# Optimization experiments

Hardware: AMD Instinct MI355X
Metric: run time of the kernel (lower is better)

The kernel has to match this reference:

```python
import math
import jax, jax.numpy as jnp
import numpy as np

H_HEADS = 8
SR = 2


def _layernorm(x, w, b, eps=1e-5):
    mu = jnp.mean(x, axis=-1, keepdims=True)
    var = jnp.mean((x - mu) ** 2, axis=-1, keepdims=True)
    return (x - mu) / jnp.sqrt(var + eps) * w + b


def _dwconv(x, w, b, pad, stride=1):
    # x: (B,C,H,W), w: (C,1,kh,kw) depthwise
    y = jax.lax.conv_general_dilated(
        x, w, (stride, stride), padding=pad,
        dimension_numbers=('NCHW', 'OIHW', 'NCHW'),
        feature_group_count=x.shape[1])
    return y + b[None, :, None, None]


def _lpu(x, w3, b3, w51, b51, w15, b15):
    # LocalPerceptionUint (act=False): x + dw3x3(x) + dw1x5(dw5x1(x))
    out = _dwconv(x, w3, b3, [(1, 1), (1, 1)])
    out2 = _dwconv(_dwconv(x, w51, b51, [(2, 2), (0, 0)]), w15, b15, [(0, 0), (2, 2)])
    return x + out + out2


def _split_halves(x, B, C, N, h, w):
    # faithful to torch: permute(0,2,1).reshape(B,C,N//2,2) then per-slice permute+reshape
    x_ = x.transpose(0, 2, 1).reshape(B, C, N // 2, 2)
    x1 = x_[..., 0].transpose(0, 2, 1).reshape(B, C, h, w)
    x2 = x_[..., 1].transpose(0, 2, 1).reshape(B, C, h, w)
    return x1, x2


def reference(x, ln_in_w, ln_in_b, ln_out_w, ln_out_b,
              lpu1_w3, lpu1_b3, lpu1_w51, lpu1_b51, lpu1_w15, lpu1_b15,
              lpu2_w3, lpu2_b3, lpu2_w51, lpu2_b51, lpu2_w15, lpu2_b15,
              q_w, q_b, kv_w, kv_b, proj_w, proj_b,
              sr1_w, sr1_b, sr2_w, sr2_b, sa_norm_w, sa_norm_b,
              mlp_w1, mlp_b1, mlp_w2, mlp_b2):
    B, N, C = x.shape
    h = int(math.isqrt(N // 2)); w = h
    dh = C // H_HEADS

    # ---- LPU on two interleaved halves ----
    x1, x2 = _split_halves(x, B, C, N, h, w)
    x1 = x1 + _lpu(x1, lpu1_w3, lpu1_b3, lpu1_w51, lpu1_b51, lpu1_w15, lpu1_b15)
    x2 = x2 + _lpu(x2, lpu2_w3, lpu2_b3, lpu2_w51, lpu2_b51, lpu2_w15, lpu2_b15)
    x = jnp.concatenate([x1, x2], axis=2).reshape(B, C, -1).transpose(0, 2, 1)  # (B,N,C)

    # ---- SelfAttention on LayerNorm(x) ----
    xa = _layernorm(x, ln_in_w, ln_in_b)
    q = (xa @ q_w.T + q_b).reshape(B, N, H_HEADS, dh).transpose(0, 2, 1, 3)  # (B,H,N,dh)

    xs1, xs2 = _split_halves(xa, B, C, N, h, w)
    xcat = jnp.concatenate([xs1, xs2], axis=2)  # (B,C,2h,w)
    pad = SR // 2
    xshift = jnp.pad(xcat, ((0, 0), (0, 0), (pad, 0), (pad, 0)))  # top/left pad
    y1 = _dwconv(xcat, sr1_w, sr1_b, [(0, 0), (0, 0)], stride=SR)
    y2 = _dwconv(xshift, sr2_w, sr2_b, [(0, 0), (0, 0)], stride=SR)
    Hs, Ws = y1.shape[2], y1.shape[3]
    y2 = y2[:, :, :Hs, :Ws]
    xk = jnp.stack([y1.reshape(B, C, -1), y2.reshape(B, C, -1)], axis=3)
    xk = xk.reshape(B, C, -1).transpose(0, 2, 1)  # (B, Nk, C), interleaved
    xk = _layernorm(xk, sa_norm_w, sa_norm_b)
    kv = (xk @ kv_w.T + kv_b).reshape(B, -1, 2, H_HEADS, dh).transpose(2, 0, 3, 1, 4)
    k, v = kv[0], kv[1]  # (B,H,Nk,dh)

    attn = jnp.einsum('bhnd,bhmd->bhnm', q, k) * (dh ** -0.5)
    M = attn.shape[-1]
    if 101 < M < 10000:  # static shape -> Python branch, matches torch gate
        topk = int(M * 0.8)
        idx = jax.lax.top_k(attn, topk)[1]  # (B,H,N,topk)
        bi = jnp.arange(B)[:, None, None, None]
        hi = jnp.arange(H_HEADS)[None, :, None, None]
        ni = jnp.arange(N)[None, None, :, None]
        mask = jnp.zeros(attn.shape, dtype=bool).at[bi, hi, ni, idx].set(True)
        attn = jnp.where(mask, attn, -jnp.inf)
    attn = jax.nn.softmax(attn, axis=-1)
    sa = jnp.einsum('bhnm,bhmd->bhnd', attn, v).transpose(0, 2, 1, 3).reshape(B, N, C)
    sa = sa @ proj_w.T + proj_b

    x = x + sa
    xm = _layernorm(x, ln_out_w, ln_out_b)
    hid = jax.nn.gelu(xm @ mlp_w1.T + mlp_b1, approximate=False)
    x = x + (hid @ mlp_w2.T + mlp_b2)
    return x


def setup_inputs():
    C = 512
    E = 4
    ks = iter(jax.random.split(jax.random.key(0), 24))

    def w(shape, std=0.02):
        return jax.random.normal(next(ks), shape, jnp.float32) * std

    inp = {"x": jax.random.normal(next(ks), (4, 2048, C), jnp.float32)}
    for nm in ("ln_in", "ln_out", "sa_norm"):
        inp[nm + "_w"] = jnp.ones((C,), jnp.float32)
        inp[nm + "_b"] = jnp.zeros((C,), jnp.float32)
    for p in ("lpu1", "lpu2"):
        inp[p + "_w3"] = w((C, 1, 3, 3))
        inp[p + "_b3"] = jnp.zeros((C,), jnp.float32)
        inp[p + "_w51"] = w((C, 1, 5, 1))
        inp[p + "_b51"] = jnp.zeros((C,), jnp.float32)
        inp[p + "_w15"] = w((C, 1, 1, 5))
        inp[p + "_b15"] = jnp.zeros((C,), jnp.float32)
    inp["q_w"] = w((C, C)); inp["q_b"] = jnp.zeros((C,), jnp.float32)
    inp["kv_w"] = w((2 * C, C)); inp["kv_b"] = jnp.zeros((2 * C,), jnp.float32)
    inp["proj_w"] = w((C, C)); inp["proj_b"] = jnp.zeros((C,), jnp.float32)
    inp["sr1_w"] = w((C, 1, SR, SR)); inp["sr1_b"] = jnp.zeros((C,), jnp.float32)
    inp["sr2_w"] = w((C, 1, SR, SR)); inp["sr2_b"] = jnp.zeros((C,), jnp.float32)
    inp["mlp_w1"] = w((E * C, C)); inp["mlp_b1"] = jnp.zeros((E * C,), jnp.float32)
    inp["mlp_w2"] = w((C, E * C)); inp["mlp_b2"] = jnp.zeros((C,), jnp.float32)
    return inp
```

## Files before the change

### kernel.cpp

```cpp
#include <hip/hip_runtime.h>
#include <stdint.h>

#define DEVI __device__ __forceinline__
typedef unsigned short u16;
typedef __attribute__((ext_vector_type(8))) short bf8v;
typedef __attribute__((ext_vector_type(4))) float f4v;

DEVI u16 f2bf(float f) {
  union { float f; uint32_t u; } v; v.f = f;
  return (u16)((v.u + 0x7fffu + ((v.u >> 16) & 1u)) >> 16);
}
DEVI float bf2f(u16 b) {
  union { uint32_t u; float f; } v; v.u = ((uint32_t)b) << 16;
  return v.f;
}
DEVI f4v mfma16(bf8v a, bf8v b, f4v c) {
  return __builtin_amdgcn_mfma_f32_16x16x32_bf16(a, b, c, 0, 0, 0);
}
DEVI void gload16(const u16* g, u16* l) {
  const auto* gp = reinterpret_cast<const uint32_t __attribute__((address_space(1)))*>(
      reinterpret_cast<uintptr_t>(g));
  auto* lp = reinterpret_cast<uint32_t __attribute__((address_space(3)))*>(
      reinterpret_cast<uintptr_t>(l));
  __builtin_amdgcn_global_load_lds(gp, lp, 16, 0, 0);
}

__global__ void cvt_kernel(const float4* __restrict__ s, ushort4* __restrict__ d, int n4) {
  int i = blockIdx.x * 256 + threadIdx.x;
  if (i < n4) {
    float4 v = s[i];
    ushort4 o; o.x = f2bf(v.x); o.y = f2bf(v.y); o.z = f2bf(v.z); o.w = f2bf(v.w);
    d[i] = o;
  }
}

__global__ __launch_bounds__(256) void lpu_kernel(
    const float* __restrict__ x, float* __restrict__ xp,
    const float* __restrict__ w3a, const float* __restrict__ b3a,
    const float* __restrict__ w51a, const float* __restrict__ b51a,
    const float* __restrict__ w15a, const float* __restrict__ b15a,
    const float* __restrict__ w3b, const float* __restrict__ b3b,
    const float* __restrict__ w51b, const float* __restrict__ b51b,
    const float* __restrict__ w15b, const float* __restrict__ b15b)
{
  __shared__ float xt[36 * 36];
  __shared__ float yt[32 * 36];
  int bid = blockIdx.x;
  int cp = bid & 511, img = (bid >> 9) & 1, b = bid >> 10;
  const float* W3  = (img ? w3b  : w3a)  + cp * 9;
  const float* W51 = (img ? w51b : w51a) + cp * 5;
  const float* W15 = (img ? w15b : w15a) + cp * 5;
  float B3  = (img ? b3b  : b3a)[cp];
  float B51 = (img ? b51b : b51a)[cp];
  float B15 = (img ? b15b : b15a)[cp];
  int t = threadIdx.x;
  for (int i = t; i < 36 * 36; i += 256) xt[i] = 0.f;
  for (int i = t; i < 32 * 36; i += 256) yt[i] = 0.f;
  __syncthreads();
  {
    int s = t * 4;
    int row = 4 * cp + 2 * (s >> 9) + img;
    float4 v = *(const float4*)(x + ((size_t)b * 2048 + row) * 512 + (s & 511));
    float* dp = &xt[(2 + (s >> 5)) * 36 + 2 + (s & 31)];
    dp[0] = v.x; dp[1] = v.y; dp[2] = v.z; dp[3] = v.w;
  }
  __syncthreads();
  float w3r[9], w51r[5], w15r[5];
  #pragma unroll
  for (int i = 0; i < 9; i++) w3r[i] = W3[i];
  #pragma unroll
  for (int i = 0; i < 5; i++) { w51r[i] = W51[i]; w15r[i] = W15[i]; }
  #pragma unroll
  for (int pp = 0; pp < 4; pp++) {
    int s = t + pp * 256;
    int i = s >> 5, j = s & 31;
    float a = B51;
    #pragma unroll
    for (int di = 0; di < 5; di++) a += w51r[di] * xt[(i + di) * 36 + 2 + j];
    yt[i * 36 + 2 + j] = a;
  }
  __syncthreads();
  #pragma unroll
  for (int pp = 0; pp < 4; pp++) {
    int s = t + pp * 256;
    int i = s >> 5, j = s & 31;
    float o = 2.f * xt[(2 + i) * 36 + 2 + j] + B3 + B15;
    #pragma unroll
    for (int di = 0; di < 3; di++)
      #pragma unroll
      for (int dj = 0; dj < 3; dj++)
        o += w3r[di * 3 + dj] * xt[(1 + i + di) * 36 + 1 + j + dj];
    #pragma unroll
    for (int dj = 0; dj < 5; dj++) o += w15r[dj] * yt[i * 36 + j + dj];
    xp[((size_t)b * 2048 + img * 1024 + s) * 512 + cp] = o;
  }
}

template<int WF32, int WBF>
__global__ __launch_bounds__(256) void ln_kernel(
    const float* __restrict__ x, const float* __restrict__ w, const float* __restrict__ bb,
    float* __restrict__ of, u16* __restrict__ ob)
{
  int row = blockIdx.x * 4 + (threadIdx.x >> 6);
  int lane = threadIdx.x & 63;
  const float4* xr = (const float4*)(x + (size_t)row * 512);
  float4 v0 = xr[lane], v1 = xr[64 + lane];
  float s = v0.x + v0.y + v0.z + v0.w + v1.x + v1.y + v1.z + v1.w;
  #pragma unroll
  for (int off = 32; off; off >>= 1) s += __shfl_xor(s, off);
  float mu = s * (1.f / 512.f);
  float q = 0.f, d;
  d = v0.x - mu; q += d * d;  d = v0.y - mu; q += d * d;
  d = v0.z - mu; q += d * d;  d = v0.w - mu; q += d * d;
  d = v1.x - mu; q += d * d;  d = v1.y - mu; q += d * d;
  d = v1.z - mu; q += d * d;  d = v1.w - mu; q += d * d;
  #pragma unroll
  for (int off = 32; off; off >>= 1) q += __shfl_xor(q, off);
  float rstd = rsqrtf(q * (1.f / 512.f) + 1e-5f);
  const float4* w4 = (const float4*)w;
  const float4* b4 = (const float4*)bb;
  float4 wa = w4[lane], wc = w4[64 + lane], ba = b4[lane], bc = b4[64 + lane];
  float4 y0, y1;
  y0.x = (v0.x - mu) * rstd * wa.x + ba.x;  y0.y = (v0.y - mu) * rstd * wa.y + ba.y;
  y0.z = (v0.z - mu) * rstd * wa.z + ba.z;  y0.w = (v0.w - mu) * rstd * wa.w + ba.w;
  y1.x = (v1.x - mu) * rstd * wc.x + bc.x;  y1.y = (v1.y - mu) * rstd * wc.y + bc.y;
  y1.z = (v1.z - mu) * rstd * wc.z + bc.z;  y1.w = (v1.w - mu) * rstd * wc.w + bc.w;
  if (WF32) {
    float4* o = (float4*)(of + (size_t)row * 512);
    o[lane] = y0; o[64 + lane] = y1;
  }
  if (WBF) {
    ushort4 p0, p1;
    p0.x = f2bf(y0.x); p0.y = f2bf(y0.y); p0.z = f2bf(y0.z); p0.w = f2bf(y0.w);
    p1.x = f2bf(y1.x); p1.y = f2bf(y1.y); p1.z = f2bf(y1.z); p1.w = f2bf(y1.w);
    ushort4* o = (ushort4*)(ob + (size_t)row * 512);
    o[lane] = p0; o[64 + lane] = p1;
  }
}

__global__ __launch_bounds__(256) void sr_kernel(
    const float* __restrict__ xa,
    const float* __restrict__ w1, const float* __restrict__ b1,
    const float* __restrict__ w2, const float* __restrict__ b2,
    float* __restrict__ xk)
{
  __shared__ float img[2048];
  int bid = blockIdx.x;
  int c = bid & 511, b = bid >> 9;
  int t = threadIdx.x;
  {
    int idx = t * 4;
    #pragma unroll
    for (int p = 0; p < 2; p++) {
      int ii = idx + p * 1024;
      int k = ii >> 9, off = ii & 511;
      int perm = (k == 1) ? 2 : ((k == 2) ? 1 : k);
      float4 v = *(const float4*)(xa + ((size_t)b * 2048 + 4 * c + perm) * 512 + off);
      *(float4*)&img[ii] = v;
    }
  }
  __syncthreads();
  float W1[4], W2[4];
  #pragma unroll
  for (int i = 0; i < 4; i++) { W1[i] = w1[c * 4 + i]; W2[i] = w2[c * 4 + i]; }
  float B1 = b1[c], B2 = b2[c];
  #pragma unroll
  for (int pp = 0; pp < 2; pp++) {
    int s = t + pp * 256;
    int p = s >> 4, q = s & 15;
    int u = 2 * p, v = 2 * q;
    float y1 = B1 + W1[0] * img[u * 32 + v]       + W1[1] * img[u * 32 + v + 1]
                  + W1[2] * img[(u + 1) * 32 + v] + W1[3] * img[(u + 1) * 32 + v + 1];
    float y2 = B2;
    #pragma unroll
    for (int di = 0; di < 2; di++)
      #pragma unroll
      for (int dj = 0; dj < 2; dj++) {
        int uu = u + di - 1, vv = v + dj - 1;
        float xv = (uu >= 0 && vv >= 0) ? img[uu * 32 + vv] : 0.f;
        y2 += W2[di * 2 + dj] * xv;
      }
    size_t base = ((size_t)b * 1024 + 2 * s) * 512 + c;
    xk[base] = y1;
    xk[base + 512] = y2;
  }
}

template<int EPI>
__global__ __launch_bounds__(256) void gemm_bt(
    const u16* __restrict__ A, const u16* __restrict__ W, const float* __restrict__ bias,
    void* __restrict__ out, const float* __restrict__ res, void* __restrict__ out2,
    int M, int N, int K)
{
  __shared__ u16 As[64 * 32];
  __shared__ u16 Bs[128 * 32];
  int tid = threadIdx.x;
  int wid = tid >> 6, lane = tid & 63;
  int wr = wid >> 1, wc = wid & 1;
  int l15 = lane & 15, lhi = lane >> 4;
  int m0 = blockIdx.y * 64, n0 = blockIdx.x * 128;
  f4v acc[2][4] = {};
  int trow = tid >> 2, tcol = (tid & 3) * 8;
  const u16* apg  = &A[(size_t)(m0 + trow) * K + tcol];
  const u16* bpg0 = &W[(size_t)(n0 + trow) * K + tcol];
  const u16* bpg1 = &W[(size_t)(n0 + 64 + trow) * K + tcol];
  u16* al  = &As[tid * 8];
  u16* bl0 = &Bs[tid * 8];
  u16* bl1 = &Bs[2048 + tid * 8];
  for (int k0 = 0; k0 < K; k0 += 32) {
    gload16(apg + k0, al);
    gload16(bpg0 + k0, bl0);
    gload16(bpg1 + k0, bl1);
    __syncthreads();
    bf8v af[2], bfr[4];
    #pragma unroll
    for (int mi = 0; mi < 2; mi++) af[mi] = *(const bf8v*)&As[(wr * 32 + mi * 16 + l15) * 32 + lhi * 8];
    #pragma unroll
    for (int ni = 0; ni < 4; ni++) bfr[ni] = *(const bf8v*)&Bs[(wc * 64 + ni * 16 + l15) * 32 + lhi * 8];
    #pragma unroll
    for (int mi = 0; mi < 2; mi++)
      #pragma unroll
      for (int ni = 0; ni < 4; ni++)
        acc[mi][ni] = mfma16(af[mi], bfr[ni], acc[mi][ni]);
    __syncthreads();
  }
  #pragma unroll
  for (int mi = 0; mi < 2; mi++) {
    #pragma unroll
    for (int ni = 0; ni < 4; ni++) {
      int col = n0 + wc * 64 + ni * 16 + l15;
      float bv = bias[col];
      #pragma unroll
      for (int r = 0; r < 4; r++) {
        int row = m0 + wr * 32 + mi * 16 + lhi * 4 + r;
        float v = acc[mi][ni][r] + bv;
        if (EPI == 0) {
          int b = row >> 11, n = row & 2047, h = col >> 6, dd = col & 63;
          ((u16*)out)[(((size_t)(b * 8 + h) * 2048) + n) * 64 + dd] = f2bf(v);
        } else if (EPI == 1) {
          int b = row >> 10, m = row & 1023;
          if (col < 512) {
            int h = col >> 6, dd = col & 63;
            ((u16*)out)[(((size_t)(b * 8 + h) * 1024) + m) * 64 + dd] = f2bf(v);
          } else {
            int h = (col - 512) >> 6, dd = col & 63;
            ((u16*)out2)[(((size_t)(b * 8 + h) * 64) + dd) * 1024 + m] = f2bf(v);
          }
        } else if (EPI == 2) {
          size_t idx = (size_t)row * N + col;
          ((float*)out)[idx] = v + res[idx];
        } else {
          float g = 0.5f * v * (1.f + erff(v * 0.70710678118f));
          ((u16*)out)[(size_t)row * N + col] = f2bf(g);
        }
      }
    }
  }
}

__global__ __launch_bounds__(256, 4) void attn_kernel(
    const u16* __restrict__ qg, const u16* __restrict__ kg,
    const u16* __restrict__ vTg, u16* __restrict__ sa)
{
  __shared__ u16 S16[16 * 1024];
  __shared__ float dn[16];
  int bid = blockIdx.x;
  int qt = bid & 127, bh = bid >> 7;
  int q0 = qt * 16;
  int tid = threadIdx.x, w = tid >> 6, lane = tid & 63;
  int l15 = lane & 15, lhi = lane >> 4;
  const u16* qbase = qg + ((size_t)bh * 2048 + q0) * 64;
  bf8v aq0 = *(const bf8v*)&qbase[l15 * 64 + lhi * 8];
  bf8v aq1 = *(const bf8v*)&qbase[l15 * 64 + 32 + lhi * 8];
  const u16* kbase = kg + (size_t)bh * 1024 * 64;
  for (int ct = 0; ct < 16; ct++) {
    int kc0 = w * 256 + ct * 16;
    const u16* kb = &kbase[(size_t)(kc0 + l15) * 64 + lhi * 8];
    bf8v bk0 = *(const bf8v*)&kb[0];
    bf8v bk1 = *(const bf8v*)&kb[32];
    f4v a = {};
    a = mfma16(aq0, bk0, a);
    a = mfma16(aq1, bk1, a);
    #pragma unroll
    for (int r = 0; r < 4; r++) {
      int row = lhi * 4 + r;
      int col = kc0 + l15;
      S16[row * 1024 + (col ^ ((row & 7) << 3))] = f2bf(a[r] * 0.125f);
    }
  }
  __syncthreads();
  for (int rr = 0; rr < 4; rr++) {
    int row = w * 4 + rr;
    int pat = (row & 7) << 3;
    float vals[16];
    #pragma unroll
    for (int j = 0; j < 16; j++) vals[j] = bf2f(S16[row * 1024 + ((j * 64 + lane) ^ pat)]);
    float vmax = vals[0], vmin = vals[0];
    #pragma unroll
    for (int j = 1; j < 16; j++) { vmax = fmaxf(vmax, vals[j]); vmin = fminf(vmin, vals[j]); }
    #pragma unroll
    for (int off = 32; off; off >>= 1) {
      vmax = fmaxf(vmax, __shfl_xor(vmax, off));
      vmin = fminf(vmin, __shfl_xor(vmin, off));
    }
    float lo = vmin, hi = vmax;
    for (int it = 0; it < 14; it++) {
      float mid = 0.5f * (lo + hi);
      int cnt = 0;
      #pragma unroll
      for (int j = 0; j < 16; j++) cnt += (int)__popcll(__ballot(vals[j] >= mid));
      if (cnt >= 819) lo = mid; else hi = mid;
    }
    float ls = 0.f;
    #pragma unroll
    for (int j = 0; j < 16; j++) {
      float pv = (vals[j] >= lo) ? __expf(vals[j] - vmax) : 0.f;
      ls += pv;
      S16[row * 1024 + ((j * 64 + lane) ^ pat)] = f2bf(pv);
    }
    #pragma unroll
    for (int off = 32; off; off >>= 1) ls += __shfl_xor(ls, off);
    if (lane == 0) dn[row] = ls;
  }
  __syncthreads();
  f4v oacc = {};
  const u16* vb = vTg + ((size_t)bh * 64 + w * 16 + l15) * 1024;
  int patp = (l15 & 7) << 3;
  for (int ks = 0; ks < 32; ks++) {
    int m0 = ks * 32;
    bf8v ap = *(const bf8v*)&S16[l15 * 1024 + ((m0 + lhi * 8) ^ patp)];
    bf8v bv = *(const bf8v*)&vb[m0 + lhi * 8];
    oacc = mfma16(ap, bv, oacc);
  }
  int b = bh >> 3, h = bh & 7;
  #pragma unroll
  for (int r = 0; r < 4; r++) {
    int row = lhi * 4 + r;
    float ov = oacc[r] / dn[row];
    sa[((size_t)b * 2048 + q0 + row) * 512 + h * 64 + w * 16 + l15] = f2bf(ov);
  }
}

extern "C" void kernel_launch(void* const* d_in, const int* in_sizes, int n_in,
                              void* d_out, int out_size, void* d_ws, size_t ws_size,
                              hipStream_t stream) {
  (void)in_sizes; (void)n_in; (void)out_size; (void)ws_size;
  const float* x        = (const float*)d_in[0];
  const float* ln_in_w  = (const float*)d_in[1];
  const float* ln_in_b  = (const float*)d_in[2];
  const float* ln_out_w = (const float*)d_in[3];
  const float* ln_out_b = (const float*)d_in[4];
  const float* sa_w     = (const float*)d_in[5];
  const float* sa_b     = (const float*)d_in[6];
  const float* q_w      = (const float*)d_in[19];
  const float* q_b      = (const float*)d_in[20];
  const float* kv_w     = (const float*)d_in[21];
  const float* kv_b     = (const float*)d_in[22];
  const float* proj_w   = (const float*)d_in[23];
  const float* proj_b   = (const float*)d_in[24];
  const float* sr1_w    = (const float*)d_in[25];
  const float* sr1_b    = (const float*)d_in[26];
  const float* sr2_w    = (const float*)d_in[27];
  const float* sr2_b    = (const float*)d_in[28];
  const float* mlp_w1   = (const float*)d_in[29];
  const float* mlp_b1   = (const float*)d_in[30];
  const float* mlp_w2   = (const float*)d_in[31];
  const float* mlp_b2   = (const float*)d_in[32];

  uint8_t* ws = (uint8_t*)d_ws;
  float* xp   = (float*)(ws + 0);
  float* xa   = (float*)(ws + 16777216);
  u16*  hid   = (u16*)(ws + 0);
  u16*  xab   = (u16*)(ws + 33554432);
  u16*  qb    = (u16*)(ws + 41943040);
  float* xk   = (float*)(ws + 50331648);
  u16*  xkb   = (u16*)(ws + 58720256);
  u16*  kb    = (u16*)(ws + 62914560);
  u16*  vTb   = (u16*)(ws + 67108864);
  u16*  sab   = (u16*)(ws + 71303168);
  float* x2   = (float*)(ws + 79691776);
  u16*  xmb   = (u16*)(ws + 96468992);
  u16*  wqb   = (u16*)(ws + 104857600);
  u16*  wkvb  = (u16*)(ws + 105381888);
  u16*  wprojb= (u16*)(ws + 106430464);
  u16*  wm1b  = (u16*)(ws + 106954752);
  u16*  wm2b  = (u16*)(ws + 109051904);

  auto cvt = [&](const float* s, u16* d, int n) {
    int n4 = n / 4;
    cvt_kernel<<<dim3((n4 + 255) / 256), dim3(256), 0, stream>>>((const float4*)s, (ushort4*)d, n4);
  };
  cvt(q_w, wqb, 512 * 512);
  cvt(kv_w, wkvb, 1024 * 512);
  cvt(proj_w, wprojb, 512 * 512);
  cvt(mlp_w1, wm1b, 2048 * 512);
  cvt(mlp_w2, wm2b, 512 * 2048);

  lpu_kernel<<<dim3(4096), dim3(256), 0, stream>>>(
      x, xp,
      (const float*)d_in[7],  (const float*)d_in[8],  (const float*)d_in[9],
      (const float*)d_in[10], (const float*)d_in[11], (const float*)d_in[12],
      (const float*)d_in[13], (const float*)d_in[14], (const float*)d_in[15],
      (const float*)d_in[16], (const float*)d_in[17], (const float*)d_in[18]);

  ln_kernel<1, 1><<<dim3(2048), dim3(256), 0, stream>>>(xp, ln_in_w, ln_in_b, xa, xab);

  sr_kernel<<<dim3(2048), dim3(256), 0, stream>>>(xa, sr1_w, sr1_b, sr2_w, sr2_b, xk);

  ln_kernel<0, 1><<<dim3(1024), dim3(256), 0, stream>>>(xk, sa_w, sa_b, nullptr, xkb);

  gemm_bt<0><<<dim3(4, 128), dim3(256), 0, stream>>>(xab, wqb, q_b, (void*)qb, nullptr, nullptr, 8192, 512, 512);
  gemm_bt<1><<<dim3(8, 64), dim3(256), 0, stream>>>(xkb, wkvb, kv_b, (void*)kb, nullptr, (void*)vTb, 4096, 1024, 512);

  attn_kernel<<<dim3(4096), dim3(256), 0, stream>>>(qb, kb, vTb, sab);

  gemm_bt<2><<<dim3(4, 128), dim3(256), 0, stream>>>(sab, wprojb, proj_b, (void*)x2, xp, nullptr, 8192, 512, 512);

  ln_kernel<0, 1><<<dim3(2048), dim3(256), 0, stream>>>(x2, ln_out_w, ln_out_b, nullptr, xmb);

  gemm_bt<3><<<dim3(16, 128), dim3(256), 0, stream>>>(xmb, wm1b, mlp_b1, (void*)hid, nullptr, nullptr, 8192, 2048, 512);
  gemm_bt<2><<<dim3(4, 128), dim3(256), 0, stream>>>(hid, wm2b, mlp_b2, d_out, x2, nullptr, 8192, 512, 2048);
}
```

Measured before the change: 486.1 us.

## Merge weight conversion into LPU kernel, fuse Q/KV GEMMs, batch softmax rows

The five weight-conversion launches are folded into the LPU kernel as extra leading blocks, and the Q and KV projections now run in one launch. The sr kernel reads the bf16 LayerNorm output instead of a separate fp32 copy, so the fp32 write of xa is dropped. The attention top-k bisection now handles four rows at once to give more instruction-level parallelism. Together these cut launch overhead and memory traffic, but the SR convolution now sees bf16-rounded inputs and the attention kernel needs more registers.

```diff
diff --git a/kernel.cpp b/kernel.cpp
--- a/kernel.cpp
+++ b/kernel.cpp
@@ -25,16 +25,9 @@
   __builtin_amdgcn_global_load_lds(gp, lp, 16, 0, 0);
 }
 
-__global__ void cvt_kernel(const float4* __restrict__ s, ushort4* __restrict__ d, int n4) {
-  int i = blockIdx.x * 256 + threadIdx.x;
-  if (i < n4) {
-    float4 v = s[i];
-    ushort4 o; o.x = f2bf(v.x); o.y = f2bf(v.y); o.z = f2bf(v.z); o.w = f2bf(v.w);
-    d[i] = o;
-  }
-}
-
-__global__ __launch_bounds__(256) void lpu_kernel(
+__global__ __launch_bounds__(256) void prep_kernel(
+    const float* __restrict__ qw, const float* __restrict__ kvw, const float* __restrict__ pw,
+    const float* __restrict__ m1w, const float* __restrict__ m2w, u16* __restrict__ wdst,
     const float* __restrict__ x, float* __restrict__ xp,
     const float* __restrict__ w3a, const float* __restrict__ b3a,
     const float* __restrict__ w51a, const float* __restrict__ b51a,
@@ -46,7 +39,21 @@
   __shared__ float xt[36 * 36];
   __shared__ float yt[32 * 36];
   int bid = blockIdx.x;
-  int cp = bid & 511, img = (bid >> 9) & 1, b = bid >> 10;
+  if (bid < 3072) {
+    int i = bid * 256 + threadIdx.x;
+    const float4* s; int local;
+    if (i < 65536)       { s = (const float4*)qw;  local = i; }
+    else if (i < 196608) { s = (const float4*)kvw; local = i - 65536; }
+    else if (i < 262144) { s = (const float4*)pw;  local = i - 196608; }
+    else if (i < 524288) { s = (const float4*)m1w; local = i - 262144; }
+    else                 { s = (const float4*)m2w; local = i - 524288; }
+    float4 v = s[local];
+    ushort4 o; o.x = f2bf(v.x); o.y = f2bf(v.y); o.z = f2bf(v.z); o.w = f2bf(v.w);
+    ((ushort4*)wdst)[i] = o;
+    return;
+  }
+  int lbid = bid - 3072;
+  int cp = lbid & 511, img = (lbid >> 9) & 1, b = lbid >> 10;
   const float* W3  = (img ? w3b  : w3a)  + cp * 9;
   const float* W51 = (img ? w51b : w51a) + cp * 5;
   const float* W15 = (img ? w15b : w15a) + cp * 5;
@@ -96,10 +103,9 @@
   }
 }
 
-template<int WF32, int WBF>
 __global__ __launch_bounds__(256) void ln_kernel(
     const float* __restrict__ x, const float* __restrict__ w, const float* __restrict__ bb,
-    float* __restrict__ of, u16* __restrict__ ob)
+    u16* __restrict__ ob)
 {
   int row = blockIdx.x * 4 + (threadIdx.x >> 6);
   int lane = threadIdx.x & 63;
@@ -120,26 +126,21 @@
   const float4* w4 = (const float4*)w;
   const float4* b4 = (const float4*)bb;
   float4 wa = w4[lane], wc = w4[64 + lane], ba = b4[lane], bc = b4[64 + lane];
-  float4 y0, y1;
-  y0.x = (v0.x - mu) * rstd * wa.x + ba.x;  y0.y = (v0.y - mu) * rstd * wa.y + ba.y;
-  y0.z = (v0.z - mu) * rstd * wa.z + ba.z;  y0.w = (v0.w - mu) * rstd * wa.w + ba.w;
-  y1.x = (v1.x - mu) * rstd * wc.x + bc.x;  y1.y = (v1.y - mu) * rstd * wc.y + bc.y;
-  y1.z = (v1.z - mu) * rstd * wc.z + bc.z;  y1.w = (v1.w - mu) * rstd * wc.w + bc.w;
-  if (WF32) {
-    float4* o = (float4*)(of + (size_t)row * 512);
-    o[lane] = y0; o[64 + lane] = y1;
-  }
-  if (WBF) {
-    ushort4 p0, p1;
-    p0.x = f2bf(y0.x); p0.y = f2bf(y0.y); p0.z = f2bf(y0.z); p0.w = f2bf(y0.w);
-    p1.x = f2bf(y1.x); p1.y = f2bf(y1.y); p1.z = f2bf(y1.z); p1.w = f2bf(y1.w);
-    ushort4* o = (ushort4*)(ob + (size_t)row * 512);
-    o[lane] = p0; o[64 + lane] = p1;
-  }
+  ushort4 p0, p1;
+  p0.x = f2bf((v0.x - mu) * rstd * wa.x + ba.x);
+  p0.y = f2bf((v0.y - mu) * rstd * wa.y + ba.y);
+  p0.z = f2bf((v0.z - mu) * rstd * wa.z + ba.z);
+  p0.w = f2bf((v0.w - mu) * rstd * wa.w + ba.w);
+  p1.x = f2bf((v1.x - mu) * rstd * wc.x + bc.x);
+  p1.y = f2bf((v1.y - mu) * rstd * wc.y + bc.y);
+  p1.z = f2bf((v1.z - mu) * rstd * wc.z + bc.z);
+  p1.w = f2bf((v1.w - mu) * rstd * wc.w + bc.w);
+  ushort4* o = (ushort4*)(ob + (size_t)row * 512);
+  o[lane] = p0; o[64 + lane] = p1;
 }
 
 __global__ __launch_bounds__(256) void sr_kernel(
-    const float* __restrict__ xa,
+    const u16* __restrict__ xab,
     const float* __restrict__ w1, const float* __restrict__ b1,
     const float* __restrict__ w2, const float* __restrict__ b2,
     float* __restrict__ xk)
@@ -149,15 +150,12 @@
   int c = bid & 511, b = bid >> 9;
   int t = threadIdx.x;
   {
-    int idx = t * 4;
-    #pragma unroll
-    for (int p = 0; p < 2; p++) {
-      int ii = idx + p * 1024;
-      int k = ii >> 9, off = ii & 511;
-      int perm = (k == 1) ? 2 : ((k == 2) ? 1 : k);
-      float4 v = *(const float4*)(xa + ((size_t)b * 2048 + 4 * c + perm) * 512 + off);
-      *(float4*)&img[ii] = v;
-    }
+    int ii = t * 8;
+    int k = ii >> 9, off = ii & 511;
+    int perm = (k == 1) ? 2 : ((k == 2) ? 1 : k);
+    bf8v v = *(const bf8v*)&xab[((size_t)b * 2048 + 4 * c + perm) * 512 + off];
+    #pragma unroll
+    for (int e = 0; e < 8; e++) img[ii + e] = bf2f(((const u16*)&v)[e]);
   }
   __syncthreads();
   float W1[4], W2[4];
@@ -187,18 +185,16 @@
 }
 
 template<int EPI>
-__global__ __launch_bounds__(256) void gemm_bt(
+DEVI void gemm_body(int bx, int by,
     const u16* __restrict__ A, const u16* __restrict__ W, const float* __restrict__ bias,
     void* __restrict__ out, const float* __restrict__ res, void* __restrict__ out2,
-    int M, int N, int K)
-{
-  __shared__ u16 As[64 * 32];
-  __shared__ u16 Bs[128 * 32];
+    int M, int N, int K, u16* As, u16* Bs)
+{
   int tid = threadIdx.x;
   int wid = tid >> 6, lane = tid & 63;
   int wr = wid >> 1, wc = wid & 1;
   int l15 = lane & 15, lhi = lane >> 4;
-  int m0 = blockIdx.y * 64, n0 = blockIdx.x * 128;
+  int m0 = by * 64, n0 = bx * 128;
   f4v acc[2][4] = {};
   int trow = tid >> 2, tcol = (tid & 3) * 8;
   const u16* apg  = &A[(size_t)(m0 + trow) * K + tcol];
@@ -258,6 +254,34 @@
   }
 }
 
+template<int EPI>
+__global__ __launch_bounds__(256) void gemm_one(
+    const u16* __restrict__ A, const u16* __restrict__ W, const float* __restrict__ bias,
+    void* __restrict__ out, const float* __restrict__ res, void* __restrict__ out2,
+    int M, int N, int K)
+{
+  __shared__ u16 As[64 * 32];
+  __shared__ u16 Bs[128 * 32];
+  gemm_body<EPI>(blockIdx.x, blockIdx.y, A, W, bias, out, res, out2, M, N, K, As, Bs);
+}
+
+__global__ __launch_bounds__(256) void gemm_qkv(
+    const u16* __restrict__ xab, const u16* __restrict__ wq, const float* __restrict__ qbias,
+    void* __restrict__ qout,
+    const u16* __restrict__ xkb, const u16* __restrict__ wkv, const float* __restrict__ kvbias,
+    void* __restrict__ kout, void* __restrict__ vout)
+{
+  __shared__ u16 As[64 * 32];
+  __shared__ u16 Bs[128 * 32];
+  int bid = blockIdx.x;
+  if (bid < 512) {
+    gemm_body<0>(bid & 3, bid >> 2, xab, wq, qbias, qout, nullptr, nullptr, 8192, 512, 512, As, Bs);
+  } else {
+    int b2 = bid - 512;
+    gemm_body<1>(b2 & 7, b2 >> 3, xkb, wkv, kvbias, kout, nullptr, vout, 4096, 1024, 512, As, Bs);
+  }
+}
+
 __global__ __launch_bounds__(256, 4) void attn_kernel(
     const u16* __restrict__ qg, const u16* __restrict__ kg,
     const u16* __restrict__ vTg, u16* __restrict__ sa)
@@ -289,38 +313,68 @@
     }
   }
   __syncthreads();
-  for (int rr = 0; rr < 4; rr++) {
-    int row = w * 4 + rr;
-    int pat = (row & 7) << 3;
-    float vals[16];
-    #pragma unroll
-    for (int j = 0; j < 16; j++) vals[j] = bf2f(S16[row * 1024 + ((j * 64 + lane) ^ pat)]);
-    float vmax = vals[0], vmin = vals[0];
-    #pragma unroll
-    for (int j = 1; j < 16; j++) { vmax = fmaxf(vmax, vals[j]); vmin = fminf(vmin, vals[j]); }
+  {
+    float vals[4][16];
+    #pragma unroll
+    for (int rr = 0; rr < 4; rr++) {
+      int row = w * 4 + rr;
+      int pat = (row & 7) << 3;
+      #pragma unroll
+      for (int j = 0; j < 16; j++)
+        vals[rr][j] = bf2f(S16[row * 1024 + ((j * 64 + lane) ^ pat)]);
+    }
+    float vmx[4], vmn[4];
+    #pragma unroll
+    for (int rr = 0; rr < 4; rr++) {
+      float a = vals[rr][0], b = vals[rr][0];
+      #pragma unroll
+      for (int j = 1; j < 16; j++) { a = fmaxf(a, vals[rr][j]); b = fminf(b, vals[rr][j]); }
+      vmx[rr] = a; vmn[rr] = b;
+    }
     #pragma unroll
     for (int off = 32; off; off >>= 1) {
-      vmax = fmaxf(vmax, __shfl_xor(vmax, off));
-      vmin = fminf(vmin, __shfl_xor(vmin, off));
-    }
-    float lo = vmin, hi = vmax;
+      #pragma unroll
+      for (int rr = 0; rr < 4; rr++) {
+        vmx[rr] = fmaxf(vmx[rr], __shfl_xor(vmx[rr], off));
+        vmn[rr] = fminf(vmn[rr], __shfl_xor(vmn[rr], off));
+      }
+    }
+    float lo[4], hi[4];
+    #pragma unroll
+    for (int rr = 0; rr < 4; rr++) { lo[rr] = vmn[rr]; hi[rr] = vmx[rr]; }
     for (int it = 0; it < 14; it++) {
-      float mid = 0.5f * (lo + hi);
-      int cnt = 0;
-      #pragma unroll
-      for (int j = 0; j < 16; j++) cnt += (int)__popcll(__ballot(vals[j] >= mid));
-      if (cnt >= 819) lo = mid; else hi = mid;
-    }
-    float ls = 0.f;
-    #pragma unroll
-    for (int j = 0; j < 16; j++) {
-      float pv = (vals[j] >= lo) ? __expf(vals[j] - vmax) : 0.f;
-      ls += pv;
-      S16[row * 1024 + ((j * 64 + lane) ^ pat)] = f2bf(pv);
-    }
-    #pragma unroll
-    for (int off = 32; off; off >>= 1) ls += __shfl_xor(ls, off);
-    if (lane == 0) dn[row] = ls;
+      #pragma unroll
+      for (int rr = 0; rr < 4; rr++) {
+        float mid = 0.5f * (lo[rr] + hi[rr]);
+        int cnt = 0;
+        #pragma unroll
+        for (int j = 0; j < 16; j++) cnt += (int)__popcll(__ballot(vals[rr][j] >= mid));
+        bool ge = (cnt >= 819);
+        lo[rr] = ge ? mid : lo[rr];
+        hi[rr] = ge ? hi[rr] : mid;
+      }
+    }
+    float ls[4] = {0.f, 0.f, 0.f, 0.f};
+    #pragma unroll
+    for (int rr = 0; rr < 4; rr++) {
+      int row = w * 4 + rr;
+      int pat = (row & 7) << 3;
+      #pragma unroll
+      for (int j = 0; j < 16; j++) {
+        float pv = (vals[rr][j] >= lo[rr]) ? __expf(vals[rr][j] - vmx[rr]) : 0.f;
+        ls[rr] += pv;
+        S16[row * 1024 + ((j * 64 + lane) ^ pat)] = f2bf(pv);
+      }
+    }
+    #pragma unroll
+    for (int off = 32; off; off >>= 1) {
+      #pragma unroll
+      for (int rr = 0; rr < 4; rr++) ls[rr] += __shfl_xor(ls[rr], off);
+    }
+    if (lane == 0) {
+      #pragma unroll
+      for (int rr = 0; rr < 4; rr++) dn[w * 4 + rr] = ls[rr];
+    }
   }
   __syncthreads();
   f4v oacc = {};
@@ -369,7 +423,6 @@
 
   uint8_t* ws = (uint8_t*)d_ws;
   float* xp   = (float*)(ws + 0);
-  float* xa   = (float*)(ws + 16777216);
   u16*  hid   = (u16*)(ws + 0);
   u16*  xab   = (u16*)(ws + 33554432);
   u16*  qb    = (u16*)(ws + 41943040);
@@ -386,38 +439,30 @@
   u16*  wm1b  = (u16*)(ws + 106954752);
   u16*  wm2b  = (u16*)(ws + 109051904);
 
-  auto cvt = [&](const float* s, u16* d, int n) {
-    int n4 = n / 4;
-    cvt_kernel<<<dim3((n4 + 255) / 256), dim3(256), 0, stream>>>((const float4*)s, (ushort4*)d, n4);
-  };
-  cvt(q_w, wqb, 512 * 512);
-  cvt(kv_w, wkvb, 1024 * 512);
-  cvt(proj_w, wprojb, 512 * 512);
-  cvt(mlp_w1, wm1b, 2048 * 512);
-  cvt(mlp_w2, wm2b, 512 * 2048);
-
-  lpu_kernel<<<dim3(4096), dim3(256), 0, stream>>>(
+
+  prep_kernel<<<dim3(7168), dim3(256), 0, stream>>>(
+      q_w, kv_w, proj_w, mlp_w1, mlp_w2, wqb,
       x, xp,
       (const float*)d_in[7],  (const float*)d_in[8],  (const float*)d_in[9],
       (const float*)d_in[10], (const float*)d_in[11], (const float*)d_in[12],
       (const float*)d_in[13], (const float*)d_in[14], (const float*)d_in[15],
       (const float*)d_in[16], (const float*)d_in[17], (const float*)d_in[18]);
 
-  ln_kernel<1, 1><<<dim3(2048), dim3(256), 0, stream>>>(xp, ln_in_w, ln_in_b, xa, xab);
-
-  sr_kernel<<<dim3(2048), dim3(256), 0, stream>>>(xa, sr1_w, sr1_b, sr2_w, sr2_b, xk);
-
-  ln_kernel<0, 1><<<dim3(1024), dim3(256), 0, stream>>>(xk, sa_w, sa_b, nullptr, xkb);
-
-  gemm_bt<0><<<dim3(4, 128), dim3(256), 0, stream>>>(xab, wqb, q_b, (void*)qb, nullptr, nullptr, 8192, 512, 512);
-  gemm_bt<1><<<dim3(8, 64), dim3(256), 0, stream>>>(xkb, wkvb, kv_b, (void*)kb, nullptr, (void*)vTb, 4096, 1024, 512);
+  ln_kernel<<<dim3(2048), dim3(256), 0, stream>>>(xp, ln_in_w, ln_in_b, xab);
+
+  sr_kernel<<<dim3(2048), dim3(256), 0, stream>>>(xab, sr1_w, sr1_b, sr2_w, sr2_b, xk);
+
+  ln_kernel<<<dim3(1024), dim3(256), 0, stream>>>(xk, sa_w, sa_b, xkb);
+
+  gemm_qkv<<<dim3(1024), dim3(256), 0, stream>>>(xab, wqb, q_b, (void*)qb,
+                                                 xkb, wkvb, kv_b, (void*)kb, (void*)vTb);
 
   attn_kernel<<<dim3(4096), dim3(256), 0, stream>>>(qb, kb, vTb, sab);
 
-  gemm_bt<2><<<dim3(4, 128), dim3(256), 0, stream>>>(sab, wprojb, proj_b, (void*)x2, xp, nullptr, 8192, 512, 512);
-
-  ln_kernel<0, 1><<<dim3(2048), dim3(256), 0, stream>>>(x2, ln_out_w, ln_out_b, nullptr, xmb);
-
-  gemm_bt<3><<<dim3(16, 128), dim3(256), 0, stream>>>(xmb, wm1b, mlp_b1, (void*)hid, nullptr, nullptr, 8192, 2048, 512);
-  gemm_bt<2><<<dim3(4, 128), dim3(256), 0, stream>>>(hid, wm2b, mlp_b2, d_out, x2, nullptr, 8192, 512, 2048);
-}
+  gemm_one<2><<<dim3(4, 128), dim3(256), 0, stream>>>(sab, wprojb, proj_b, (void*)x2, xp, nullptr, 8192, 512, 512);
+
+  ln_kernel<<<dim3(2048), dim3(256), 0, stream>>>(x2, ln_out_w, ln_out_b, xmb);
+
+  gemm_one<3><<<dim3(16, 128), dim3(256), 0, stream>>>(xmb, wm1b, mlp_b1, (void*)hid, nullptr, nullptr, 8192, 2048, 512);
+  gemm_one<2><<<dim3(4, 128), dim3(256), 0, stream>>>(hid, wm2b, mlp_b2, d_out, x2, nullptr, 8192, 512, 2048);
+}
```

Result: slower. 524.1 us (+7.8%).
